# Optimization experiments

Measured on AMD Instinct MI355X. Metric: run time of the kernel, lower is better.

Reference implementation:

```python
import jax, jax.numpy as jnp
import numpy as np

B, T, D = 4, 2048, 1024  # batch, seq, latent_dim == attn_dim
H = 16                   # n_heads
HS = D // H              # head_size = 64
FF = 4 * D               # ffn hidden
EPS = 1e-5


def layernorm(x, g, b):
    mu = jnp.mean(x, axis=-1, keepdims=True)
    var = jnp.mean(jnp.square(x - mu), axis=-1, keepdims=True)
    return (x - mu) * jax.lax.rsqrt(var + EPS) * g + b


def setup_inputs() -> dict:
    key = jax.random.key(0)
    ks = jax.random.split(key, 12)
    s = lambda fan_in: 1.0 / np.sqrt(fan_in)
    return {
        "x": jax.random.normal(ks[0], (B, T, D), dtype=jnp.float32),
        "ln1_g": jnp.ones((D,), jnp.float32),
        "ln1_b": jnp.zeros((D,), jnp.float32),
        "W_ap": jax.random.normal(ks[1], (D, D), jnp.float32) * s(D),
        "b_ap": jnp.zeros((D,), jnp.float32),
        "W_qkv": jax.random.normal(ks[2], (D, 3 * D), jnp.float32) * s(D),
        "b_qkv": jnp.zeros((3 * D,), jnp.float32),
        "W_proj": jax.random.normal(ks[3], (D, D), jnp.float32) * s(D),
        "b_proj": jnp.zeros((D,), jnp.float32),
        "ln2_g": jnp.ones((D,), jnp.float32),
        "ln2_b": jnp.zeros((D,), jnp.float32),
        "W1": jax.random.normal(ks[4], (D, FF), jnp.float32) * s(D),
        "b1": jnp.zeros((FF,), jnp.float32),
        "W2": jax.random.normal(ks[5], (FF, D), jnp.float32) * s(FF),
        "b2": jnp.zeros((D,), jnp.float32),
    }


def block_fwd(x, ln1_g, ln1_b, W_ap, b_ap, W_qkv, b_qkv, W_proj, b_proj,
              ln2_g, ln2_b, W1, b1, W2, b2):
    # --- self attention branch ---
    a = layernorm(x, ln1_g, ln1_b)
    a = a @ W_ap + b_ap                       # [B,T,D]
    qkv = a @ W_qkv + b_qkv                   # [B,T,3D]
    q, k, v = jnp.split(qkv, 3, axis=-1)
    q = q.reshape(B, T, H, HS).transpose(0, 2, 1, 3)  # [B,H,T,HS]
    k = k.reshape(B, T, H, HS).transpose(0, 2, 1, 3)
    v = v.reshape(B, T, H, HS).transpose(0, 2, 1, 3)
    scores = jnp.einsum('bhqd,bhkd->bhqk', q, k) * (1.0 / np.sqrt(HS))
    probs = jax.nn.softmax(scores, axis=-1)   # full [B,H,T,T], no causal mask (as in source)
    o = jnp.einsum('bhqk,bhkd->bhqd', probs, v)
    o = o.transpose(0, 2, 1, 3).reshape(B, T, D)
    o = o @ W_proj + b_proj
    h = x + o
    # --- ffn branch: GELU(LayerNorm(h)) -> Linear -> GELU -> Linear ---
    f = jax.nn.gelu(layernorm(h, ln2_g, ln2_b), approximate=False)
    f = jax.nn.gelu(f @ W1 + b1, approximate=False) @ W2 + b2
    return h + f


def reference(x, ln1_g, ln1_b, W_ap, b_ap, W_qkv, b_qkv, W_proj, b_proj,
              ln2_g, ln2_b, W1, b1, W2, b2):
    return block_fwd(x, ln1_g, ln1_b, W_ap, b_ap, W_qkv, b_qkv, W_proj, b_proj,
                     ln2_g, ln2_b, W1, b1, W2, b2)
```

## Files before the change

kernel.cpp:

```cpp
#include <hip/hip_runtime.h>
#include <hip/hip_bf16.h>
#include <math.h>


typedef unsigned short u16;
typedef __attribute__((ext_vector_type(8))) short s16x8;
typedef __attribute__((ext_vector_type(4))) float f32x4;

__device__ __forceinline__ u16 f2bf(float f) {
    unsigned u = __float_as_uint(f);
    u += 0x7fffu + ((u >> 16) & 1u);
    return (u16)(u >> 16);
}
__device__ __forceinline__ unsigned pkbf2(float a, float b) {
    float2 t; t.x = a; t.y = b;
    __hip_bfloat162 r = __float22bfloat162_rn(t);
    return *(unsigned*)&r;
}
__device__ __forceinline__ float bf2f(short s) {
    return __uint_as_float(((unsigned)(unsigned short)s) << 16);
}
__device__ __forceinline__ float gelu_f(float v) {
    float u = v * v;
    float x = v * fmaf(0.0356774081f, u, 0.7978845608f);
    float t = __builtin_amdgcn_exp2f(x * 2.885390082f);
    float th = fmaf(-2.0f, __builtin_amdgcn_rcpf(t + 1.0f), 1.0f);
    float hv = 0.5f * v;
    return fmaf(hv, th, hv);
}
__device__ __forceinline__ void glds16(const u16* g, u16* l) {
    __builtin_amdgcn_global_load_lds(
        (const __attribute__((address_space(1))) void*)g,
        (__attribute__((address_space(3))) void*)l, 16, 0, 0);
}
__device__ __forceinline__ void barfence() {
    __builtin_amdgcn_s_barrier();
    asm volatile("" ::: "memory");
}

__global__ __launch_bounds__(256) void transpose_f32_bf16(
    const float* __restrict__ in, u16* __restrict__ out, int K, int N) {
    __shared__ float t[32][33];
    int n0 = blockIdx.x * 32, k0 = blockIdx.y * 32;
    int c = threadIdx.x, r0 = threadIdx.y;
#pragma unroll
    for (int i = 0; i < 4; i++) {
        int r = r0 + i * 8;
        t[r][c] = in[(size_t)(k0 + r) * N + n0 + c];
    }
    __syncthreads();
#pragma unroll
    for (int i = 0; i < 4; i++) {
        int r = r0 + i * 8;
        out[(size_t)(n0 + r) * K + k0 + c] = f2bf(t[c][r]);
    }
}

template <bool GELU>
__global__ __launch_bounds__(256) void ln_kernel(
    const float* __restrict__ x, const float* __restrict__ g,
    const float* __restrict__ bt, u16* __restrict__ out) {
    const int D = 1024;
    int row = blockIdx.x;
    float4 v = reinterpret_cast<const float4*>(x + (size_t)row * D)[threadIdx.x];
    float s = v.x + v.y + v.z + v.w;
    float s2 = v.x * v.x + v.y * v.y + v.z * v.z + v.w * v.w;
#pragma unroll
    for (int off = 32; off > 0; off >>= 1) {
        s += __shfl_down(s, off);
        s2 += __shfl_down(s2, off);
    }
    __shared__ float red[8];
    int wid = threadIdx.x >> 6;
    if ((threadIdx.x & 63) == 0) { red[wid] = s; red[wid + 4] = s2; }
    __syncthreads();
    s = red[0] + red[1] + red[2] + red[3];
    s2 = red[4] + red[5] + red[6] + red[7];
    float mu = s * (1.0f / 1024.0f);
    float var = s2 * (1.0f / 1024.0f) - mu * mu;
    float rstd = rsqrtf(var + 1e-5f);
    float4 gg = reinterpret_cast<const float4*>(g)[threadIdx.x];
    float4 bb = reinterpret_cast<const float4*>(bt)[threadIdx.x];
    float o0 = (v.x - mu) * rstd * gg.x + bb.x;
    float o1 = (v.y - mu) * rstd * gg.y + bb.y;
    float o2 = (v.z - mu) * rstd * gg.z + bb.z;
    float o3 = (v.w - mu) * rstd * gg.w + bb.w;
    if (GELU) { o0 = gelu_f(o0); o1 = gelu_f(o1); o2 = gelu_f(o2); o3 = gelu_f(o3); }
    uint2 o;
    o.x = pkbf2(o0, o1); o.y = pkbf2(o2, o3);
    reinterpret_cast<uint2*>(out + (size_t)row * D)[threadIdx.x] = o;
}

template <int OUT_BF16, int ACT_GELU, int HAS_RES>
__global__ __launch_bounds__(512, 2) void gemm_kernel(
    const u16* __restrict__ A, const u16* __restrict__ BT,
    const float* __restrict__ bias, const float* __restrict__ res,
    void* __restrict__ outp, int M, int N, int K) {
    __shared__ u16 As[2 * 256 * 64];
    __shared__ u16 Bs[2 * 256 * 64];
    const int nwg = gridDim.x * gridDim.y;
    int wg = blockIdx.y * gridDim.x + blockIdx.x;
    wg = (wg & 7) * (nwg >> 3) + (wg >> 3);
    const int m0 = (wg / gridDim.x) * 256, n0 = (wg % gridDim.x) * 256;
    const int tid = threadIdx.x;
    const int w = tid >> 6, lane = tid & 63, l16 = lane & 15, quad = lane >> 4;
    const int wm = w >> 2, wn = w & 3;

    const int lrow = lane >> 3;
    const int lcol = ((lane & 7) ^ lrow) * 8;
    const u16* Ag = A + (size_t)(m0 + w * 16 + lrow) * K + lcol;
    const u16* Bg = BT + (size_t)(n0 + w * 16 + lrow) * K + lcol;

    const int cx0 = (quad ^ (l16 & 7)) * 8;
    const int cx1 = cx0 ^ 32;

    f32x4 acc[2][2][4][2] = {};
    const int nt = K >> 6;

#define STAGE_A(AH, BUF, KK)                                              \
    do {                                                                  \
        const u16* _s = Ag + (size_t)((AH) * 128) * K + (KK);             \
        u16* _d = As + (BUF) * 16384 + ((AH) * 128 + w * 16) * 64;        \
        glds16(_s, _d);                                                   \
        glds16(_s + (size_t)8 * K, _d + 512);                             \
    } while (0)
#define STAGE_B(BH, BUF, KK)                                              \
    do {                                                                  \
        const u16* _s = Bg + (size_t)((BH) * 128) * K + (KK);             \
        u16* _d = Bs + (BUF) * 16384 + ((BH) * 128 + w * 16) * 64;        \
        glds16(_s, _d);                                                   \
        glds16(_s + (size_t)8 * K, _d + 512);                             \
    } while (0)

    STAGE_A(0, 0, 0);
    STAGE_B(0, 0, 0);
    STAGE_B(1, 0, 0);
    STAGE_A(1, 0, 0);
    asm volatile("s_waitcnt vmcnt(4)" ::: "memory");
    barfence();

    s16x8 af[4][2], bfA[2][2], bfB[2][2];

    for (int t = 0; t < nt; ++t) {
        const int cur = t & 1, nxt = cur ^ 1;
        const int kk = (t + 1) << 6;
        const bool pre = (t + 1) < nt;
        const u16* Ab = As + cur * 16384;
        const u16* Bb = Bs + cur * 16384;

#pragma unroll
        for (int i = 0; i < 4; ++i) {
            const u16* p = Ab + (wm * 64 + i * 16 + l16) * 64;
            af[i][0] = *(const s16x8*)(p + cx0);
            af[i][1] = *(const s16x8*)(p + cx1);
        }
#pragma unroll
        for (int j = 0; j < 2; ++j) {
            const u16* p = Bb + (wn * 32 + j * 16 + l16) * 64;
            bfA[j][0] = *(const s16x8*)(p + cx0);
            bfA[j][1] = *(const s16x8*)(p + cx1);
        }
        if (pre) STAGE_A(0, nxt, kk);
        barfence();
        asm volatile("s_waitcnt lgkmcnt(0)" ::: "memory");
        __builtin_amdgcn_sched_barrier(0);
        __builtin_amdgcn_s_setprio(1);
#pragma unroll
        for (int kd = 0; kd < 2; ++kd)
#pragma unroll
            for (int i = 0; i < 4; ++i)
#pragma unroll
                for (int j = 0; j < 2; ++j)
                    acc[0][0][i][j] = __builtin_amdgcn_mfma_f32_16x16x32_bf16(
                        af[i][kd], bfA[j][kd], acc[0][0][i][j], 0, 0, 0);
        __builtin_amdgcn_s_setprio(0);
        if (pre) asm volatile("s_waitcnt vmcnt(4)" ::: "memory");
        else     asm volatile("s_waitcnt vmcnt(2)" ::: "memory");
        barfence();

#pragma unroll
        for (int j = 0; j < 2; ++j) {
            const u16* p = Bb + (128 + wn * 32 + j * 16 + l16) * 64;
            bfB[j][0] = *(const s16x8*)(p + cx0);
            bfB[j][1] = *(const s16x8*)(p + cx1);
        }
        if (pre) STAGE_B(0, nxt, kk);
        barfence();
        asm volatile("s_waitcnt lgkmcnt(0)" ::: "memory");
        __builtin_amdgcn_sched_barrier(0);
        __builtin_amdgcn_s_setprio(1);
#pragma unroll
        for (int kd = 0; kd < 2; ++kd)
#pragma unroll
            for (int i = 0; i < 4; ++i)
#pragma unroll
                for (int j = 0; j < 2; ++j)
                    acc[0][1][i][j] = __builtin_amdgcn_mfma_f32_16x16x32_bf16(
                        af[i][kd], bfB[j][kd], acc[0][1][i][j], 0, 0, 0);
        __builtin_amdgcn_s_setprio(0);
        if (pre) asm volatile("s_waitcnt vmcnt(4)" ::: "memory");
        else     asm volatile("s_waitcnt vmcnt(0)" ::: "memory");
        barfence();

#pragma unroll
        for (int i = 0; i < 4; ++i) {
            const u16* p = Ab + (128 + wm * 64 + i * 16 + l16) * 64;
            af[i][0] = *(const s16x8*)(p + cx0);
            af[i][1] = *(const s16x8*)(p + cx1);
        }
        if (pre) STAGE_B(1, nxt, kk);
        barfence();
        asm volatile("s_waitcnt lgkmcnt(0)" ::: "memory");
        __builtin_amdgcn_sched_barrier(0);
        __builtin_amdgcn_s_setprio(1);
#pragma unroll
        for (int kd = 0; kd < 2; ++kd)
#pragma unroll
            for (int i = 0; i < 4; ++i)
#pragma unroll
                for (int j = 0; j < 2; ++j)
                    acc[1][1][i][j] = __builtin_amdgcn_mfma_f32_16x16x32_bf16(
                        af[i][kd], bfB[j][kd], acc[1][1][i][j], 0, 0, 0);
        __builtin_amdgcn_s_setprio(0);
        barfence();

        if (pre) STAGE_A(1, nxt, kk);
        __builtin_amdgcn_sched_barrier(0);
        __builtin_amdgcn_s_setprio(1);
#pragma unroll
        for (int kd = 0; kd < 2; ++kd)
#pragma unroll
            for (int i = 0; i < 4; ++i)
#pragma unroll
                for (int j = 0; j < 2; ++j)
                    acc[1][0][i][j] = __builtin_amdgcn_mfma_f32_16x16x32_bf16(
                        af[i][kd], bfA[j][kd], acc[1][0][i][j], 0, 0, 0);
        __builtin_amdgcn_s_setprio(0);
        if (pre) {
            asm volatile("s_waitcnt vmcnt(4)" ::: "memory");
            barfence();
        }
    }
#undef STAGE_A
#undef STAGE_B

    float bv[2][2];
#pragma unroll
    for (int bh = 0; bh < 2; ++bh)
#pragma unroll
        for (int j = 0; j < 2; ++j)
            bv[bh][j] = bias[n0 + bh * 128 + wn * 32 + j * 16 + l16];

#pragma unroll
    for (int ah = 0; ah < 2; ++ah)
#pragma unroll
        for (int i = 0; i < 4; ++i) {
            int rowb = m0 + ah * 128 + wm * 64 + i * 16 + quad * 4;
#pragma unroll
            for (int bh = 0; bh < 2; ++bh)
#pragma unroll
                for (int j = 0; j < 2; ++j) {
                    int col = n0 + bh * 128 + wn * 32 + j * 16 + l16;
#pragma unroll
                    for (int r = 0; r < 4; ++r) {
                        float v = acc[ah][bh][i][j][r] + bv[bh][j];
                        if (ACT_GELU) v = gelu_f(v);
                        size_t idx = (size_t)(rowb + r) * N + col;
                        if (HAS_RES) v += res[idx];
                        if (OUT_BF16) ((u16*)outp)[idx] = f2bf(v);
                        else          ((float*)outp)[idx] = v;
                    }
                }
        }
}

template <int OUT_BF16, int HAS_RES, int SPLIT_V>
__global__ __launch_bounds__(512, 2) void gemm_n128(
    const u16* __restrict__ A, const u16* __restrict__ BT,
    const float* __restrict__ bias, const float* __restrict__ res,
    void* __restrict__ outp, u16* __restrict__ vtg, int M, int N, int K) {
    __shared__ u16 As[3 * 256 * 64];
    __shared__ u16 Bs[3 * 128 * 64];
    const int nwg = gridDim.x * gridDim.y;
    int wg = blockIdx.y * gridDim.x + blockIdx.x;
    wg = (wg & 7) * (nwg >> 3) + (wg >> 3);
    const int m0 = (wg / gridDim.x) * 256, n0 = (wg % gridDim.x) * 128;
    const int tid = threadIdx.x;
    const int w = tid >> 6, lane = tid & 63, l16 = lane & 15, quad = lane >> 4;
    const int wm = w >> 1, wn = w & 1;

    const int lrow = lane >> 3;
    const int lcol = ((lane & 7) ^ lrow) * 8;
    const u16* Ag = A + (size_t)(m0 + w * 16 + lrow) * K + lcol;
    const u16* Bg = BT + (size_t)(n0 + w * 16 + lrow) * K + lcol;

    const int cx0 = (quad ^ (l16 & 7)) * 8;
    const int cx1 = cx0 ^ 32;

    f32x4 acc[4][4] = {};
    const int nt = K >> 6;

#define NSTAGE_A(BUF, KK)                                                 \
    do {                                                                  \
        const u16* _s = Ag + (KK);                                        \
        u16* _d = As + (BUF) * 16384 + (w * 16) * 64;                     \
        glds16(_s, _d);                                                   \
        glds16(_s + (size_t)8 * K, _d + 512);                             \
        glds16(_s + (size_t)128 * K, _d + 8192);                          \
        glds16(_s + (size_t)136 * K, _d + 8192 + 512);                    \
    } while (0)
#define NSTAGE_B(BUF, KK)                                                 \
    do {                                                                  \
        const u16* _s = Bg + (KK);                                        \
        u16* _d = Bs + (BUF) * 8192 + (w * 16) * 64;                      \
        glds16(_s, _d);                                                   \
        glds16(_s + (size_t)8 * K, _d + 512);                             \
    } while (0)

    NSTAGE_A(0, 0);
    NSTAGE_B(0, 0);
    NSTAGE_A(1, 64);
    NSTAGE_B(1, 64);
    asm volatile("s_waitcnt vmcnt(6)" ::: "memory");
    barfence();

    s16x8 af[4][2], bf[2][2];
    int cur = 0, b2 = 2;
    for (int t = 0; t < nt; ++t) {
        const bool pre2 = (t + 2) < nt;
        const u16* Ab = As + cur * 16384;
        const u16* Bb = Bs + cur * 8192;
        const int kk2 = (t + 2) << 6;

#pragma unroll
        for (int i = 0; i < 4; ++i) {
            const u16* p = Ab + (wm * 64 + i * 16 + l16) * 64;
            af[i][0] = *(const s16x8*)(p + cx0);
            af[i][1] = *(const s16x8*)(p + cx1);
        }
#pragma unroll
        for (int j = 0; j < 2; ++j) {
            const u16* p = Bb + (wn * 64 + j * 16 + l16) * 64;
            bf[j][0] = *(const s16x8*)(p + cx0);
            bf[j][1] = *(const s16x8*)(p + cx1);
        }
        if (pre2) NSTAGE_A(b2, kk2);
        barfence();
        asm volatile("s_waitcnt lgkmcnt(0)" ::: "memory");
        __builtin_amdgcn_sched_barrier(0);
        __builtin_amdgcn_s_setprio(1);
#pragma unroll
        for (int kd = 0; kd < 2; ++kd)
#pragma unroll
            for (int i = 0; i < 4; ++i)
#pragma unroll
                for (int j = 0; j < 2; ++j)
                    acc[i][j] = __builtin_amdgcn_mfma_f32_16x16x32_bf16(
                        af[i][kd], bf[j][kd], acc[i][j], 0, 0, 0);
        __builtin_amdgcn_s_setprio(0);
        barfence();

#pragma unroll
        for (int j = 0; j < 2; ++j) {
            const u16* p = Bb + (wn * 64 + 32 + j * 16 + l16) * 64;
            bf[j][0] = *(const s16x8*)(p + cx0);
            bf[j][1] = *(const s16x8*)(p + cx1);
        }
        if (pre2) NSTAGE_B(b2, kk2);
        barfence();
        asm volatile("s_waitcnt lgkmcnt(0)" ::: "memory");
        __builtin_amdgcn_sched_barrier(0);
        __builtin_amdgcn_s_setprio(1);
#pragma unroll
        for (int kd = 0; kd < 2; ++kd)
#pragma unroll
            for (int i = 0; i < 4; ++i)
#pragma unroll
                for (int j = 0; j < 2; ++j)
                    acc[i][2 + j] = __builtin_amdgcn_mfma_f32_16x16x32_bf16(
                        af[i][kd], bf[j][kd], acc[i][2 + j], 0, 0, 0);
        __builtin_amdgcn_s_setprio(0);
        if (pre2)               asm volatile("s_waitcnt vmcnt(6)" ::: "memory");
        else if (t + 1 < nt)    asm volatile("s_waitcnt vmcnt(0)" ::: "memory");
        if (t + 1 < nt) barfence();

        cur = (cur == 2) ? 0 : cur + 1;
        b2 = (b2 == 2) ? 0 : b2 + 1;
    }
#undef NSTAGE_A
#undef NSTAGE_B

    float bv[4];
#pragma unroll
    for (int j = 0; j < 4; ++j) bv[j] = bias[n0 + wn * 64 + j * 16 + l16];

    if (SPLIT_V && n0 >= 2048) {
#pragma unroll
        for (int i = 0; i < 4; ++i) {
            int rowb = m0 + wm * 64 + i * 16 + quad * 4;
            int bb = rowb >> 11, tt = rowb & 2047;
            int tp = (tt & ~63) | (tt & 0x23) | ((tt & 0x0C) << 1) | ((tt & 0x10) >> 2);
#pragma unroll
            for (int j = 0; j < 4; ++j) {
                int vcol = n0 + wn * 64 + j * 16 + l16 - 2048;
                uint2 pk;
                pk.x = pkbf2(acc[i][j][0] + bv[j], acc[i][j][1] + bv[j]);
                pk.y = pkbf2(acc[i][j][2] + bv[j], acc[i][j][3] + bv[j]);
                *(uint2*)&vtg[((size_t)bb * 1024 + vcol) * 2048 + tp] = pk;
            }
        }
    } else {
#pragma unroll
        for (int i = 0; i < 4; ++i) {
            int rowb = m0 + wm * 64 + i * 16 + quad * 4;
#pragma unroll
            for (int j = 0; j < 4; ++j) {
                int col = n0 + wn * 64 + j * 16 + l16;
#pragma unroll
                for (int r = 0; r < 4; ++r) {
                    float v = acc[i][j][r] + bv[j];
                    size_t idx = (size_t)(rowb + r) * N + col;
                    if (HAS_RES) v += res[idx];
                    if (OUT_BF16) ((u16*)outp)[idx] = f2bf(v);
                    else          ((float*)outp)[idx] = v;
                }
            }
        }
    }
}

__global__ __launch_bounds__(256) void knorm_kernel(
    const u16* __restrict__ qkv, float* __restrict__ maxkn) {
    const int T = 2048, D3 = 3072;
    int bh = blockIdx.x, b = bh >> 4, h = bh & 15;
    const u16* kg = qkv + (size_t)b * T * D3 + 1024 + h * 64;
    float mx = 0.f;
#pragma unroll
    for (int i = 0; i < 8; i++) {
        const u16* kp = kg + (size_t)(threadIdx.x + i * 256) * D3;
        float ss = 0.f;
#pragma unroll
        for (int c = 0; c < 8; c++) {
            s16x8 v = *(const s16x8*)(kp + c * 8);
#pragma unroll
            for (int j = 0; j < 8; j++) { float f = bf2f(v[j]); ss = fmaf(f, f, ss); }
        }
        mx = fmaxf(mx, ss);
    }
#pragma unroll
    for (int off = 32; off > 0; off >>= 1) mx = fmaxf(mx, __shfl_down(mx, off));
    __shared__ float red[4];
    if ((threadIdx.x & 63) == 0) red[threadIdx.x >> 6] = mx;
    __syncthreads();
    if (threadIdx.x == 0)
        maxkn[bh] = sqrtf(fmaxf(fmaxf(red[0], red[1]), fmaxf(red[2], red[3])));
}

__global__ __launch_bounds__(256, 4) void attn_kernel(
    const u16* __restrict__ qkv, const u16* __restrict__ vtg,
    const float* __restrict__ maxkn, u16* __restrict__ o) {
    const int T = 2048, D3 = 3072, Dm = 1024;
    const int bh = blockIdx.x, qb = blockIdx.y;
    const int b = bh >> 4, h = bh & 15;
    const int tid = threadIdx.x;
    const int w = tid >> 6, lane = tid & 63, l16 = lane & 15, quad = lane >> 4;
    const size_t tokbase = (size_t)b * T;
    const float s2 = 0.125f * 1.44269504088896f;

    __shared__ u16 Ks[2][64 * 64];
    __shared__ u16 Vts[2][64 * 64];

    s16x8 bq[2][2];
    float m2[2];
    const float kn = maxkn[bh];
#pragma unroll
    for (int qs = 0; qs < 2; qs++) {
        int qrow = qb * 128 + w * 32 + qs * 16 + l16;
        const u16* qp = qkv + (tokbase + qrow) * D3 + h * 64 + quad * 8;
        bq[qs][0] = *(const s16x8*)qp;
        bq[qs][1] = *(const s16x8*)(qp + 32);
        float ss = 0.f;
#pragma unroll
        for (int kd = 0; kd < 2; kd++)
#pragma unroll
            for (int j = 0; j < 8; j++) {
                float v = bf2f(bq[qs][kd][j]); ss = fmaf(v, v, ss);
            }
        ss += __shfl_xor(ss, 16);
        ss += __shfl_xor(ss, 32);
        m2[qs] = sqrtf(ss) * kn * s2;
    }

    f32x4 acc_ot[2][4] = {};
    float lp[2] = {0.f, 0.f};

    const int lr = lane >> 3;
    const int lcs = ((lane & 7) ^ lr) * 8;
    const u16* kgl = qkv + tokbase * D3 + 1024 + h * 64 + (size_t)(w * 16 + lr) * D3 + lcs;
    const u16* vgl = vtg + ((size_t)b * 1024 + h * 64 + w * 16 + lr) * T + lcs;

    const int cq0 = (quad ^ (l16 & 7)) * 8;
    const int cq1 = cq0 ^ 32;

#define ASTAGE(BUF, KT)                                                   \
    do {                                                                  \
        const u16* _k = kgl + (size_t)(KT) * 64 * D3;                     \
        glds16(_k, &Ks[BUF][(w * 16) * 64]);                              \
        glds16(_k + (size_t)8 * D3, &Ks[BUF][(w * 16 + 8) * 64]);         \
        const u16* _v = vgl + (KT) * 64;                                  \
        glds16(_v, &Vts[BUF][(w * 16) * 64]);                             \
        glds16(_v + (size_t)8 * T, &Vts[BUF][(w * 16 + 8) * 64]);         \
    } while (0)

    ASTAGE(0, 0);
    asm volatile("s_waitcnt vmcnt(0)" ::: "memory");
    barfence();

    for (int kt = 0; kt < 32; kt++) {
        const int cur = kt & 1;
        if (kt + 1 < 32) ASTAGE(cur ^ 1, kt + 1);

        f32x4 st[2][4] = {};
        __builtin_amdgcn_s_setprio(1);
#pragma unroll
        for (int kd = 0; kd < 2; kd++)
#pragma unroll
            for (int kb = 0; kb < 4; kb++) {
                s16x8 ak = *(const s16x8*)&Ks[cur][(kb * 16 + l16) * 64 + (kd ? cq1 : cq0)];
#pragma unroll
                for (int qs = 0; qs < 2; qs++)
                    st[qs][kb] = __builtin_amdgcn_mfma_f32_16x16x32_bf16(
                        ak, bq[qs][kd], st[qs][kb], 0, 0, 0);
            }
        __builtin_amdgcn_s_setprio(0);

        unsigned px[2][4], py[2][4];
#pragma unroll
        for (int qs = 0; qs < 2; qs++) {
            float acc_l = 0.f;
#pragma unroll
            for (int kb = 0; kb < 4; kb++) {
#pragma unroll
                for (int r = 0; r < 4; r++) {
                    float pv = __builtin_amdgcn_exp2f(fmaf(st[qs][kb][r], s2, -m2[qs]));
                    st[qs][kb][r] = pv;
                    acc_l += pv;
                }
                px[qs][kb] = pkbf2(st[qs][kb][0], st[qs][kb][1]);
                py[qs][kb] = pkbf2(st[qs][kb][2], st[qs][kb][3]);
            }
            lp[qs] += acc_l;
        }

#pragma unroll
        for (int kk = 0; kk < 2; kk++) {
            s16x8 bp[2];
#pragma unroll
            for (int qs = 0; qs < 2; qs++) {
                union { s16x8 v; unsigned u[4]; } bb;
                bb.u[0] = px[qs][2 * kk];
                bb.u[1] = py[qs][2 * kk];
                bb.u[2] = px[qs][2 * kk + 1];
                bb.u[3] = py[qs][2 * kk + 1];
                bp[qs] = bb.v;
            }
            __builtin_amdgcn_s_setprio(1);
#pragma unroll
            for (int dt = 0; dt < 4; dt++) {
                s16x8 av = *(const s16x8*)&Vts[cur][(dt * 16 + l16) * 64 + (kk ? cq1 : cq0)];
#pragma unroll
                for (int qs = 0; qs < 2; qs++)
                    acc_ot[qs][dt] = __builtin_amdgcn_mfma_f32_16x16x32_bf16(
                        av, bp[qs], acc_ot[qs][dt], 0, 0, 0);
            }
            __builtin_amdgcn_s_setprio(0);
        }

        if (kt + 1 < 32) asm volatile("s_waitcnt vmcnt(0)" ::: "memory");
        barfence();
    }
#undef ASTAGE

#pragma unroll
    for (int qs = 0; qs < 2; qs++) {
        float l = lp[qs];
        l += __shfl_xor(l, 16);
        l += __shfl_xor(l, 32);
        float inv = 1.0f / l;
        int token = qb * 128 + w * 32 + qs * 16 + l16;
#pragma unroll
        for (int dt = 0; dt < 4; dt++) {
            uint2 pk;
            pk.x = pkbf2(acc_ot[qs][dt][0] * inv, acc_ot[qs][dt][1] * inv);
            pk.y = pkbf2(acc_ot[qs][dt][2] * inv, acc_ot[qs][dt][3] * inv);
            *(uint2*)&o[(tokbase + token) * Dm + h * 64 + dt * 16 + quad * 4] = pk;
        }
    }
}

extern "C" void kernel_launch(void* const* d_in, const int* in_sizes, int n_in,
                              void* d_out, int out_size, void* d_ws, size_t ws_size,
                              hipStream_t stream) {
    const int M = 8192;
    const int D = 1024, D3 = 3072, FF = 4096;

    const float* x      = (const float*)d_in[0];
    const float* ln1_g  = (const float*)d_in[1];
    const float* ln1_b  = (const float*)d_in[2];
    const float* W_ap   = (const float*)d_in[3];
    const float* b_ap   = (const float*)d_in[4];
    const float* W_qkv  = (const float*)d_in[5];
    const float* b_qkv  = (const float*)d_in[6];
    const float* W_proj = (const float*)d_in[7];
    const float* b_proj = (const float*)d_in[8];
    const float* ln2_g  = (const float*)d_in[9];
    const float* ln2_b  = (const float*)d_in[10];
    const float* W1     = (const float*)d_in[11];
    const float* b1     = (const float*)d_in[12];
    const float* W2     = (const float*)d_in[13];
    const float* b2     = (const float*)d_in[14];

    char* p = (char*)d_ws;
    auto carve = [&](size_t bytes) { char* r = p; p += (bytes + 255) & ~(size_t)255; return r; };
    u16*   WapT   = (u16*)carve((size_t)D * D * 2);
    u16*   WqkvT  = (u16*)carve((size_t)D * D3 * 2);
    u16*   WprojT = (u16*)carve((size_t)D * D * 2);
    u16*   W1T    = (u16*)carve((size_t)D * FF * 2);
    u16*   W2T    = (u16*)carve((size_t)FF * D * 2);
    u16*   aln    = (u16*)carve((size_t)M * D * 2);
    u16*   a1     = (u16*)carve((size_t)M * D * 2);
    u16*   qkvb   = (u16*)carve((size_t)M * D3 * 2);
    float* hbuf   = (float*)carve((size_t)M * D * 4);
    u16*   f1     = (u16*)carve((size_t)M * FF * 2);
    float* maxkn  = (float*)carve(64 * 4);
    u16* gbuf = aln;
    u16* obuf = a1;
    u16* vtg  = f1;

    dim3 tb(32, 8);
    transpose_f32_bf16<<<dim3(D / 32, D / 32), tb, 0, stream>>>(W_ap, WapT, D, D);
    transpose_f32_bf16<<<dim3(D3 / 32, D / 32), tb, 0, stream>>>(W_qkv, WqkvT, D, D3);
    transpose_f32_bf16<<<dim3(D / 32, D / 32), tb, 0, stream>>>(W_proj, WprojT, D, D);
    transpose_f32_bf16<<<dim3(FF / 32, D / 32), tb, 0, stream>>>(W1, W1T, D, FF);
    transpose_f32_bf16<<<dim3(D / 32, FF / 32), tb, 0, stream>>>(W2, W2T, FF, D);

    ln_kernel<false><<<M, 256, 0, stream>>>(x, ln1_g, ln1_b, aln);
    gemm_n128<1, 0, 0><<<dim3(D / 128, M / 256), 512, 0, stream>>>(
        aln, WapT, b_ap, nullptr, a1, nullptr, M, D, D);
    gemm_n128<1, 0, 1><<<dim3(D3 / 128, M / 256), 512, 0, stream>>>(
        a1, WqkvT, b_qkv, nullptr, qkvb, vtg, M, D3, D);
    knorm_kernel<<<64, 256, 0, stream>>>(qkvb, maxkn);
    attn_kernel<<<dim3(64, 16), 256, 0, stream>>>(qkvb, vtg, maxkn, obuf);
    gemm_n128<0, 1, 0><<<dim3(D / 128, M / 256), 512, 0, stream>>>(
        obuf, WprojT, b_proj, x, hbuf, nullptr, M, D, D);
    ln_kernel<true><<<M, 256, 0, stream>>>(hbuf, ln2_g, ln2_b, gbuf);
    gemm_kernel<1, 1, 0><<<dim3(FF / 256, M / 256), 512, 0, stream>>>(
        gbuf, W1T, b1, nullptr, f1, M, FF, D);
    gemm_n128<0, 1, 0><<<dim3(D / 128, M / 256), 512, 0, stream>>>(
        f1, W2T, b2, hbuf, (float*)d_out, nullptr, M, D, FF);
}
```

Baseline: 533.3 us.

## Collapse ping-pong GEMM phases into one LDS read and MFMA burst per k-step

Both GEMM kernels now read every A/B fragment from LDS at the start of each k-step, issue all global-to-LDS prefetches for the next tile at once, and run all MFMAs in one block without the intermediate barriers and lgkmcnt waits. This removes several workgroup barriers per iteration and is meant to give the scheduler a longer stretch of MFMAs to overlap with loads. The cost is more fragment registers (af0/af1, bfA/bfB), which can lower occupancy. In the 256x256 kernel the prefetch wait is also tightened to vmcnt(0), which reduces how much of the next tile's load can stay in flight across the barrier. The LDS waits now rely on compiler-inserted waitcnts rather than explicit sched_barrier ordering, and writes into the next buffer depend on the barrier at the end of the previous iteration.

```diff
diff --git a/kernel.cpp b/kernel.cpp
--- a/kernel.cpp
+++ b/kernel.cpp
@@ -136,10 +136,10 @@
     STAGE_B(0, 0, 0);
     STAGE_B(1, 0, 0);
     STAGE_A(1, 0, 0);
-    asm volatile("s_waitcnt vmcnt(4)" ::: "memory");
+    asm volatile("s_waitcnt vmcnt(0)" ::: "memory");
     barfence();
 
-    s16x8 af[4][2], bfA[2][2], bfB[2][2];
+    s16x8 af0[4][2], af1[4][2], bfA[2][2], bfB[2][2];
 
     for (int t = 0; t < nt; ++t) {
         const int cur = t & 1, nxt = cur ^ 1;
@@ -149,46 +149,44 @@
         const u16* Bb = Bs + cur * 16384;
 
 #pragma unroll
-        for (int i = 0; i < 4; ++i) {
-            const u16* p = Ab + (wm * 64 + i * 16 + l16) * 64;
-            af[i][0] = *(const s16x8*)(p + cx0);
-            af[i][1] = *(const s16x8*)(p + cx1);
-        }
-#pragma unroll
         for (int j = 0; j < 2; ++j) {
             const u16* p = Bb + (wn * 32 + j * 16 + l16) * 64;
             bfA[j][0] = *(const s16x8*)(p + cx0);
             bfA[j][1] = *(const s16x8*)(p + cx1);
         }
-        if (pre) STAGE_A(0, nxt, kk);
-        barfence();
-        asm volatile("s_waitcnt lgkmcnt(0)" ::: "memory");
-        __builtin_amdgcn_sched_barrier(0);
-        __builtin_amdgcn_s_setprio(1);
-#pragma unroll
-        for (int kd = 0; kd < 2; ++kd)
-#pragma unroll
-            for (int i = 0; i < 4; ++i)
-#pragma unroll
-                for (int j = 0; j < 2; ++j)
-                    acc[0][0][i][j] = __builtin_amdgcn_mfma_f32_16x16x32_bf16(
-                        af[i][kd], bfA[j][kd], acc[0][0][i][j], 0, 0, 0);
-        __builtin_amdgcn_s_setprio(0);
-        if (pre) asm volatile("s_waitcnt vmcnt(4)" ::: "memory");
-        else     asm volatile("s_waitcnt vmcnt(2)" ::: "memory");
-        barfence();
-
+#pragma unroll
+        for (int i = 0; i < 4; ++i) {
+            const u16* p = Ab + (wm * 64 + i * 16 + l16) * 64;
+            af0[i][0] = *(const s16x8*)(p + cx0);
+            af0[i][1] = *(const s16x8*)(p + cx1);
+        }
 #pragma unroll
         for (int j = 0; j < 2; ++j) {
             const u16* p = Bb + (128 + wn * 32 + j * 16 + l16) * 64;
             bfB[j][0] = *(const s16x8*)(p + cx0);
             bfB[j][1] = *(const s16x8*)(p + cx1);
         }
-        if (pre) STAGE_B(0, nxt, kk);
-        barfence();
-        asm volatile("s_waitcnt lgkmcnt(0)" ::: "memory");
-        __builtin_amdgcn_sched_barrier(0);
+#pragma unroll
+        for (int i = 0; i < 4; ++i) {
+            const u16* p = Ab + (128 + wm * 64 + i * 16 + l16) * 64;
+            af1[i][0] = *(const s16x8*)(p + cx0);
+            af1[i][1] = *(const s16x8*)(p + cx1);
+        }
+        if (pre) {
+            STAGE_A(0, nxt, kk);
+            STAGE_B(0, nxt, kk);
+            STAGE_B(1, nxt, kk);
+            STAGE_A(1, nxt, kk);
+        }
         __builtin_amdgcn_s_setprio(1);
+#pragma unroll
+        for (int kd = 0; kd < 2; ++kd)
+#pragma unroll
+            for (int i = 0; i < 4; ++i)
+#pragma unroll
+                for (int j = 0; j < 2; ++j)
+                    acc[0][0][i][j] = __builtin_amdgcn_mfma_f32_16x16x32_bf16(
+                        af0[i][kd], bfA[j][kd], acc[0][0][i][j], 0, 0, 0);
 #pragma unroll
         for (int kd = 0; kd < 2; ++kd)
 #pragma unroll
@@ -196,23 +194,7 @@
 #pragma unroll
                 for (int j = 0; j < 2; ++j)
                     acc[0][1][i][j] = __builtin_amdgcn_mfma_f32_16x16x32_bf16(
-                        af[i][kd], bfB[j][kd], acc[0][1][i][j], 0, 0, 0);
-        __builtin_amdgcn_s_setprio(0);
-        if (pre) asm volatile("s_waitcnt vmcnt(4)" ::: "memory");
-        else     asm volatile("s_waitcnt vmcnt(0)" ::: "memory");
-        barfence();
-
-#pragma unroll
-        for (int i = 0; i < 4; ++i) {
-            const u16* p = Ab + (128 + wm * 64 + i * 16 + l16) * 64;
-            af[i][0] = *(const s16x8*)(p + cx0);
-            af[i][1] = *(const s16x8*)(p + cx1);
-        }
-        if (pre) STAGE_B(1, nxt, kk);
-        barfence();
-        asm volatile("s_waitcnt lgkmcnt(0)" ::: "memory");
-        __builtin_amdgcn_sched_barrier(0);
-        __builtin_amdgcn_s_setprio(1);
+                        af0[i][kd], bfB[j][kd], acc[0][1][i][j], 0, 0, 0);
 #pragma unroll
         for (int kd = 0; kd < 2; ++kd)
 #pragma unroll
@@ -220,13 +202,7 @@
 #pragma unroll
                 for (int j = 0; j < 2; ++j)
                     acc[1][1][i][j] = __builtin_amdgcn_mfma_f32_16x16x32_bf16(
-                        af[i][kd], bfB[j][kd], acc[1][1][i][j], 0, 0, 0);
-        __builtin_amdgcn_s_setprio(0);
-        barfence();
-
-        if (pre) STAGE_A(1, nxt, kk);
-        __builtin_amdgcn_sched_barrier(0);
-        __builtin_amdgcn_s_setprio(1);
+                        af1[i][kd], bfB[j][kd], acc[1][1][i][j], 0, 0, 0);
 #pragma unroll
         for (int kd = 0; kd < 2; ++kd)
 #pragma unroll
@@ -234,10 +210,10 @@
 #pragma unroll
                 for (int j = 0; j < 2; ++j)
                     acc[1][0][i][j] = __builtin_amdgcn_mfma_f32_16x16x32_bf16(
-                        af[i][kd], bfA[j][kd], acc[1][0][i][j], 0, 0, 0);
+                        af1[i][kd], bfA[j][kd], acc[1][0][i][j], 0, 0, 0);
         __builtin_amdgcn_s_setprio(0);
         if (pre) {
-            asm volatile("s_waitcnt vmcnt(4)" ::: "memory");
+            asm volatile("s_waitcnt vmcnt(0)" ::: "memory");
             barfence();
         }
     }
@@ -324,7 +300,7 @@
     asm volatile("s_waitcnt vmcnt(6)" ::: "memory");
     barfence();
 
-    s16x8 af[4][2], bf[2][2];
+    s16x8 af[4][2], bfA[2][2], bfB[2][2];
     int cur = 0, b2 = 2;
     for (int t = 0; t < nt; ++t) {
         const bool pre2 = (t + 2) < nt;
@@ -333,6 +309,12 @@
         const int kk2 = (t + 2) << 6;
 
 #pragma unroll
+        for (int j = 0; j < 2; ++j) {
+            const u16* p = Bb + (wn * 64 + j * 16 + l16) * 64;
+            bfA[j][0] = *(const s16x8*)(p + cx0);
+            bfA[j][1] = *(const s16x8*)(p + cx1);
+        }
+#pragma unroll
         for (int i = 0; i < 4; ++i) {
             const u16* p = Ab + (wm * 64 + i * 16 + l16) * 64;
             af[i][0] = *(const s16x8*)(p + cx0);
@@ -340,14 +322,14 @@
         }
 #pragma unroll
         for (int j = 0; j < 2; ++j) {
-            const u16* p = Bb + (wn * 64 + j * 16 + l16) * 64;
-            bf[j][0] = *(const s16x8*)(p + cx0);
-            bf[j][1] = *(const s16x8*)(p + cx1);
-        }
-        if (pre2) NSTAGE_A(b2, kk2);
-        barfence();
-        asm volatile("s_waitcnt lgkmcnt(0)" ::: "memory");
-        __builtin_amdgcn_sched_barrier(0);
+            const u16* p = Bb + (wn * 64 + 32 + j * 16 + l16) * 64;
+            bfB[j][0] = *(const s16x8*)(p + cx0);
+            bfB[j][1] = *(const s16x8*)(p + cx1);
+        }
+        if (pre2) {
+            NSTAGE_A(b2, kk2);
+            NSTAGE_B(b2, kk2);
+        }
         __builtin_amdgcn_s_setprio(1);
 #pragma unroll
         for (int kd = 0; kd < 2; ++kd)
@@ -356,21 +338,7 @@
 #pragma unroll
                 for (int j = 0; j < 2; ++j)
                     acc[i][j] = __builtin_amdgcn_mfma_f32_16x16x32_bf16(
-                        af[i][kd], bf[j][kd], acc[i][j], 0, 0, 0);
-        __builtin_amdgcn_s_setprio(0);
-        barfence();
-
-#pragma unroll
-        for (int j = 0; j < 2; ++j) {
-            const u16* p = Bb + (wn * 64 + 32 + j * 16 + l16) * 64;
-            bf[j][0] = *(const s16x8*)(p + cx0);
-            bf[j][1] = *(const s16x8*)(p + cx1);
-        }
-        if (pre2) NSTAGE_B(b2, kk2);
-        barfence();
-        asm volatile("s_waitcnt lgkmcnt(0)" ::: "memory");
-        __builtin_amdgcn_sched_barrier(0);
-        __builtin_amdgcn_s_setprio(1);
+                        af[i][kd], bfA[j][kd], acc[i][j], 0, 0, 0);
 #pragma unroll
         for (int kd = 0; kd < 2; ++kd)
 #pragma unroll
@@ -378,7 +346,7 @@
 #pragma unroll
                 for (int j = 0; j < 2; ++j)
                     acc[i][2 + j] = __builtin_amdgcn_mfma_f32_16x16x32_bf16(
-                        af[i][kd], bf[j][kd], acc[i][2 + j], 0, 0, 0);
+                        af[i][kd], bfB[j][kd], acc[i][2 + j], 0, 0, 0);
         __builtin_amdgcn_s_setprio(0);
         if (pre2)               asm volatile("s_waitcnt vmcnt(6)" ::: "memory");
         else if (t + 1 < nt)    asm volatile("s_waitcnt vmcnt(0)" ::: "memory");
```

After: 534.0 us. No clear change (+0.1%).
